# Performance work log

Measured on AMD Instinct MI355X. Metric: run time of the kernel, lower is better.

The kernel has to match this reference:

```python
import jax, jax.numpy as jnp
import numpy as np

D = 512       # hidden_size (attention defaults hardcode 512)
N = 8         # num_heads
H = D // N    # depth per head = 64
FF = 2048     # FFN filter size (hardcoded)
EPS = 1e-6


def _layer_norm(x, gamma, beta):
    # matches functional layer_norm: biased variance, eps inside sqrt
    mean = jnp.mean(x, axis=-1, keepdims=True)
    var = jnp.mean((x - mean) ** 2, axis=-1, keepdims=True)
    return gamma * ((x - mean) / jnp.sqrt(var + EPS)) + beta


def setup_inputs() -> dict:
    key = jax.random.key(0)
    ks = jax.random.split(key, 12)
    B, S = 8, 1024
    s = lambda k, shape, scale: jax.random.normal(k, shape, jnp.float32) * scale
    return {
        "inputs": s(ks[0], (B, S, D), 1.0),
        "attention_bias": jnp.zeros((B, 1, 1, S), jnp.float32),
        "ln1_g": jnp.ones((D,), jnp.float32),
        "ln1_b": jnp.zeros((D,), jnp.float32),
        "wq": s(ks[1], (D, N, H), D ** -0.5),
        "wk": s(ks[2], (D, N, H), D ** -0.5),
        "wv": s(ks[3], (D, N, H), D ** -0.5),
        "wo": s(ks[4], (N, H, D), D ** -0.5),
        "ln2_g": jnp.ones((D,), jnp.float32),
        "ln2_b": jnp.zeros((D,), jnp.float32),
        "w1": s(ks[5], (D, FF), D ** -0.5),
        "b1": jnp.zeros((FF,), jnp.float32),
        "w2": s(ks[6], (FF, D), FF ** -0.5),
        "b2": jnp.zeros((D,), jnp.float32),
    }


def reference(inputs, attention_bias, ln1_g, ln1_b, wq, wk, wv, wo,
              ln2_g, ln2_b, w1, b1, w2, b2):
    # --- self-attention block (pre-LN, residual) ---
    y = _layer_norm(inputs, ln1_g, ln1_b)
    q = jnp.einsum('bsd,dnh->bsnh', y, wq) * (H ** -0.5)
    k = jnp.einsum('bsd,dnh->bsnh', y, wk)
    v = jnp.einsum('bsd,dnh->bsnh', y, wv)
    # logits[b,n,f,t] = sum_h k[b,t,n,h] * q[b,f,n,h]
    logits = jnp.einsum('btnh,bfnh->bnft', k, q) + attention_bias
    weights = jax.nn.softmax(logits, axis=3)
    attn = jnp.einsum('bnft,btnh->bfnh', weights, v)
    attn_out = jnp.einsum('bfnh,nhd->bfd', attn, wo)
    x = inputs + attn_out

    # --- FFN block (pre-LN, residual) ---
    y2 = _layer_norm(x, ln2_g, ln2_b)
    h = jax.nn.relu(jnp.einsum('bsd,df->bsf', y2, w1) + b1)
    ffn_out = jnp.einsum('bsf,fd->bsd', h, w2) + b2
    return x + ffn_out
```

## Files before the change

### kernel.cpp

```cpp
#include <hip/hip_runtime.h>
#include <stdint.h>

typedef unsigned short u16;
typedef __attribute__((ext_vector_type(8))) __bf16 bf16x8;
typedef __attribute__((ext_vector_type(4))) float f32x4;

__device__ __forceinline__ float bf2f(u16 u) {
    union { unsigned int i; float f; } c; c.i = ((unsigned int)u) << 16; return c.f;
}
__device__ __forceinline__ u16 f2bf(float f) {
    union { float f; unsigned int i; } c; c.f = f;
    unsigned int u = c.i;
    u += 0x7FFFu + ((u >> 16) & 1u);
    return (u16)(u >> 16);
}
__device__ __forceinline__ bool sniff_f32(const unsigned* probe) {
    return probe && ((*probe & 0xFFFFu) == 0u);
}
__device__ __forceinline__ float lde(const void* p, size_t i, bool isf32) {
    return isf32 ? ((const float*)p)[i] : bf2f(((const u16*)p)[i]);
}
__device__ __forceinline__ void g2lds16(const void* g, void* l) {
    __builtin_amdgcn_global_load_lds(
        (__attribute__((address_space(1))) void*)(uintptr_t)g,
        (__attribute__((address_space(3))) void*)(unsigned int)(uintptr_t)l,
        16, 0, 0);
}

__global__ void prep_weights(const void* __restrict__ wq, const void* __restrict__ wk,
                             const void* __restrict__ wv, const void* __restrict__ wo,
                             const void* __restrict__ w1, const void* __restrict__ w2,
                             u16* __restrict__ wqkvT, u16* __restrict__ woT,
                             u16* __restrict__ w1T, u16* __restrict__ w2T,
                             const unsigned* probe) {
    __shared__ u16 t[32][33];
    const bool isf32 = sniff_f32(probe);
    const int id = blockIdx.x;
    const void* src; u16* dst; int R, C, cb, rb; float scale = 1.f;
    if (id < 1024) {
        const int which = id >> 8, tl = id & 255;
        R = 512; C = 512; cb = (tl & 15) * 32; rb = (tl >> 4) * 32;
        if (which == 0)      { src = wq; dst = wqkvT;              scale = 0.125f; }
        else if (which == 1) { src = wk; dst = wqkvT + 512 * 512; }
        else if (which == 2) { src = wv; dst = wqkvT + 1024 * 512; }
        else                 { src = wo; dst = woT; }
    } else if (id < 2048) {
        const int tl = id - 1024; src = w1; dst = w1T; R = 512; C = 2048;
        cb = (tl & 63) * 32; rb = (tl >> 6) * 32;
    } else {
        const int tl = id - 2048; src = w2; dst = w2T; R = 2048; C = 512;
        cb = (tl & 15) * 32; rb = (tl >> 4) * 32;
    }
    const int tx = threadIdx.x, ty = threadIdx.y;
#pragma unroll
    for (int i = 0; i < 4; i++)
        t[ty + i * 8][tx] = f2bf(lde(src, (size_t)(rb + ty + i * 8) * C + cb + tx, isf32));
    __syncthreads();
#pragma unroll
    for (int i = 0; i < 4; i++) {
        float v = bf2f(t[tx][ty + i * 8]) * scale;
        dst[(size_t)(cb + ty + i * 8) * R + rb + tx] = f2bf(v);
    }
}

__global__ __launch_bounds__(256) void ln_any(const void* __restrict__ x,
                                              const void* __restrict__ gw,
                                              const void* __restrict__ bw,
                                              u16* __restrict__ y,
                                              const unsigned* probe_x,
                                              const unsigned* probe_gb) {
    const bool xf32 = sniff_f32(probe_x);
    const bool gf32 = sniff_f32(probe_gb);
    const int lane = threadIdx.x & 63, wave = threadIdx.x >> 6;
    const int r = blockIdx.x * 4 + wave;
    union U8 { uint4 v; u16 s[8]; };
    float xs[8];
    if (xf32) {
        const float4* xr = (const float4*)((const float*)x + (size_t)r * 512 + lane * 8);
        float4 p0 = xr[0], p1 = xr[1];
        xs[0]=p0.x; xs[1]=p0.y; xs[2]=p0.z; xs[3]=p0.w;
        xs[4]=p1.x; xs[5]=p1.y; xs[6]=p1.z; xs[7]=p1.w;
    } else {
        U8 xu; xu.v = *(const uint4*)((const u16*)x + (size_t)r * 512 + lane * 8);
#pragma unroll
        for (int j = 0; j < 8; j++) xs[j] = bf2f(xu.s[j]);
    }
    float s1 = 0.f, s2 = 0.f;
#pragma unroll
    for (int j = 0; j < 8; j++) { s1 += xs[j]; s2 += xs[j] * xs[j]; }
#pragma unroll
    for (int d = 1; d < 64; d <<= 1) { s1 += __shfl_xor(s1, d); s2 += __shfl_xor(s2, d); }
    const float mean = s1 * (1.f / 512.f);
    const float var = s2 * (1.f / 512.f) - mean * mean;
    const float rstd = rsqrtf(var + 1e-6f);
    float gs[8], bs[8];
    if (gf32) {
        const float4* gr = (const float4*)((const float*)gw + lane * 8);
        const float4* br = (const float4*)((const float*)bw + lane * 8);
        float4 g0 = gr[0], g1 = gr[1], b0 = br[0], b1 = br[1];
        gs[0]=g0.x; gs[1]=g0.y; gs[2]=g0.z; gs[3]=g0.w; gs[4]=g1.x; gs[5]=g1.y; gs[6]=g1.z; gs[7]=g1.w;
        bs[0]=b0.x; bs[1]=b0.y; bs[2]=b0.z; bs[3]=b0.w; bs[4]=b1.x; bs[5]=b1.y; bs[6]=b1.z; bs[7]=b1.w;
    } else {
        U8 gu; gu.v = *(const uint4*)((const u16*)gw + lane * 8);
        U8 bu; bu.v = *(const uint4*)((const u16*)bw + lane * 8);
#pragma unroll
        for (int j = 0; j < 8; j++) { gs[j] = bf2f(gu.s[j]); bs[j] = bf2f(bu.s[j]); }
    }
    union U8 ou;
#pragma unroll
    for (int j = 0; j < 8; j++)
        ou.s[j] = f2bf(gs[j] * ((xs[j] - mean) * rstd) + bs[j]);
    *(uint4*)(y + (size_t)r * 512 + lane * 8) = ou.v;
}

template <int EPI>
__global__ __launch_bounds__(256, 2) void gemm_bt(const u16* __restrict__ A,
                                                  const u16* __restrict__ Bt,
                                                  const void* __restrict__ bias,
                                                  const void* __restrict__ res,
                                                  void* __restrict__ out,
                                                  u16* __restrict__ out2,
                                                  const unsigned* probe,
                                                  int M, int N, int K) {
    __shared__ __align__(16) u16 lA[128 * 32];
    __shared__ __align__(16) u16 lB[128 * 32];
    const int tid = threadIdx.x, wave = tid >> 6, lane = tid & 63;
    const int m0 = blockIdx.x * 128, n0 = blockIdx.y * 128;
    const int wm = (wave >> 1) * 64, wn = (wave & 1) * 64;
    const int row = lane & 15, quad = lane >> 4;
    f32x4 acc[4][4];
#pragma unroll
    for (int i = 0; i < 4; i++)
#pragma unroll
        for (int j = 0; j < 4; j++) acc[i][j] = (f32x4){0.f, 0.f, 0.f, 0.f};
    const u16* Ab = A + (size_t)m0 * K;
    const u16* Bb = Bt + (size_t)n0 * K;
    const int ch0 = wave, ch1 = wave + 4;
    const int e0 = ch0 * 64 + lane, e1 = ch1 * 64 + lane;
    const int r0 = e0 >> 2, c0 = (e0 & 3) * 8;
    const int r1 = e1 >> 2, c1 = (e1 & 3) * 8;
    for (int k0 = 0; k0 < K; k0 += 32) {
        __syncthreads();
        g2lds16(Ab + (size_t)r0 * K + k0 + c0, (char*)lA + ch0 * 1024);
        g2lds16(Bb + (size_t)r0 * K + k0 + c0, (char*)lB + ch0 * 1024);
        g2lds16(Ab + (size_t)r1 * K + k0 + c1, (char*)lA + ch1 * 1024);
        g2lds16(Bb + (size_t)r1 * K + k0 + c1, (char*)lB + ch1 * 1024);
        __syncthreads();
        bf16x8 af[4], bfr[4];
#pragma unroll
        for (int t = 0; t < 4; t++) {
            af[t]  = *(const bf16x8*)(lA + (wm + t * 16 + row) * 32 + quad * 8);
            bfr[t] = *(const bf16x8*)(lB + (wn + t * 16 + row) * 32 + quad * 8);
        }
#pragma unroll
        for (int i = 0; i < 4; i++)
#pragma unroll
            for (int j = 0; j < 4; j++)
                acc[i][j] = __builtin_amdgcn_mfma_f32_16x16x32_bf16(af[i], bfr[j], acc[i][j], 0, 0, 0);
    }
    const bool isf32 = sniff_f32(probe);
#pragma unroll
    for (int i = 0; i < 4; i++) {
        const int gm = m0 + wm + i * 16 + quad * 4;
#pragma unroll
        for (int j = 0; j < 4; j++) {
            const int gn = n0 + wn + j * 16 + row;
            float bv = 0.f;
            if (EPI == 2 || EPI == 3) bv = lde(bias, gn, isf32);
#pragma unroll
            for (int r = 0; r < 4; r++) {
                float v = acc[i][j][r];
                const int gmr = gm + r;
                size_t idx = (size_t)gmr * N + gn;
                if (EPI == 1) {
                    ((u16*)out)[idx] = f2bf(v + lde(res, idx, isf32));
                } else if (EPI == 2) {
                    v += bv;
                    ((u16*)out)[idx] = f2bf(v > 0.f ? v : 0.f);
                } else if (EPI == 3) {
                    v += bv + bf2f(((const u16*)res)[idx]);
                    if (isf32) ((float*)out)[idx] = v;
                    else       ((u16*)out)[idx] = f2bf(v);
                } else {
                    if (gn < 1024) {
                        ((u16*)out)[(size_t)gmr * 1024 + gn] = f2bf(v);
                    } else {
                        const int j2 = gn - 1024, n = j2 >> 6, h2 = j2 & 63;
                        const int b = gmr >> 10, t = gmr & 1023;
                        out2[(((size_t)b * 8 + n) * 64 + h2) * 1024 + t] = f2bf(v);
                    }
                }
            }
        }
    }
}

__global__ __launch_bounds__(256, 2) void attn_fused(const u16* __restrict__ qk,
                                                     const u16* __restrict__ vT,
                                                     const void* __restrict__ biasp,
                                                     u16* __restrict__ attn,
                                                     const unsigned* probe) {
    __shared__ __align__(16) u16 lQ[64 * 64];
    __shared__ __align__(16) u16 lK[128 * 64];
    __shared__ __align__(16) u16 lV[64 * 128];
    const bool isf32 = sniff_f32(probe);
    const int tid = threadIdx.x, wave = tid >> 6, lane = tid & 63;
    const int row = lane & 15, quad = lane >> 4;
    const int bn = blockIdx.x, b = bn >> 3, n = bn & 7;
    const int f0 = blockIdx.y * 64;
    const u16* Qg = qk + (size_t)(b * 1024 + f0) * 1024 + n * 64;
    const u16* Kg = qk + (size_t)(b * 1024) * 1024 + 512 + n * 64;
    const u16* Vg = vT + (size_t)bn * 65536;

#pragma unroll
    for (int j = 0; j < 2; j++) {
        const int ch = wave * 2 + j, e = ch * 64 + lane;
        const int rq = e >> 3, cq = ((e & 7) ^ (rq & 7)) * 8;
        g2lds16(Qg + (size_t)rq * 1024 + cq, (char*)lQ + ch * 1024);
    }
    float m_i = -1e30f, l_i = 0.f;
    f32x4 oacc[4];
#pragma unroll
    for (int h = 0; h < 4; h++) oacc[h] = (f32x4){0.f, 0.f, 0.f, 0.f};

    for (int t0 = 0; t0 < 1024; t0 += 128) {
        __syncthreads();
#pragma unroll
        for (int j = 0; j < 4; j++) {
            const int ch = wave * 4 + j, e = ch * 64 + lane;
            const int rk = e >> 3, ck = ((e & 7) ^ (rk & 7)) * 8;
            g2lds16(Kg + (size_t)(t0 + rk) * 1024 + ck, (char*)lK + ch * 1024);
            const int rv = e >> 4, cv = ((e & 15) ^ (rv & 7)) * 8;
            g2lds16(Vg + (size_t)rv * 1024 + t0 + cv, (char*)lV + ch * 1024);
        }
        __syncthreads();
        f32x4 s[8];
#pragma unroll
        for (int nt = 0; nt < 8; nt++) s[nt] = (f32x4){0.f, 0.f, 0.f, 0.f};
        const int fr = wave * 16 + row;
        bf16x8 bq[2];
#pragma unroll
        for (int ks = 0; ks < 2; ks++)
            bq[ks] = *(const bf16x8*)(lQ + fr * 64 + (((ks * 4 + quad) ^ (fr & 7)) * 8));
#pragma unroll
        for (int nt = 0; nt < 8; nt++) {
            const int tr = nt * 16 + row;
#pragma unroll
            for (int ks = 0; ks < 2; ks++) {
                bf16x8 ak = *(const bf16x8*)(lK + tr * 64 + (((ks * 4 + quad) ^ (tr & 7)) * 8));
                s[nt] = __builtin_amdgcn_mfma_f32_16x16x32_bf16(ak, bq[ks], s[nt], 0, 0, 0);
            }
        }
        float mx = -1e30f;
#pragma unroll
        for (int nt = 0; nt < 8; nt++) {
            const size_t bidx = (size_t)b * 1024 + t0 + nt * 16 + quad * 4;
            float bv4[4];
            if (isf32) {
                float4 t4 = *(const float4*)((const float*)biasp + bidx);
                bv4[0] = t4.x; bv4[1] = t4.y; bv4[2] = t4.z; bv4[3] = t4.w;
            } else {
                union { uint2 v; u16 s[4]; } bu;
                bu.v = *(const uint2*)((const u16*)biasp + bidx);
#pragma unroll
                for (int r = 0; r < 4; r++) bv4[r] = bf2f(bu.s[r]);
            }
#pragma unroll
            for (int r = 0; r < 4; r++) {
                s[nt][r] += bv4[r];
                mx = fmaxf(mx, s[nt][r]);
            }
        }
        mx = fmaxf(mx, __shfl_xor(mx, 16));
        mx = fmaxf(mx, __shfl_xor(mx, 32));
        const float mn = fmaxf(m_i, mx);
        const float alpha = __expf(m_i - mn);
        float rs = 0.f;
#pragma unroll
        for (int nt = 0; nt < 8; nt++)
#pragma unroll
            for (int r = 0; r < 4; r++) {
                float p = __expf(s[nt][r] - mn);
                s[nt][r] = p;
                rs += p;
            }
        rs += __shfl_xor(rs, 16);
        rs += __shfl_xor(rs, 32);
        l_i = l_i * alpha + rs;
        m_i = mn;
#pragma unroll
        for (int h = 0; h < 4; h++)
#pragma unroll
            for (int r = 0; r < 4; r++) oacc[h][r] *= alpha;
#pragma unroll
        for (int ks = 0; ks < 4; ks++) {
            unsigned pw[4];
#pragma unroll
            for (int g = 0; g < 2; g++) {
                pw[g * 2 + 0] = (unsigned)f2bf(s[ks * 2 + g][0]) | ((unsigned)f2bf(s[ks * 2 + g][1]) << 16);
                pw[g * 2 + 1] = (unsigned)f2bf(s[ks * 2 + g][2]) | ((unsigned)f2bf(s[ks * 2 + g][3]) << 16);
            }
            union { unsigned u[4]; bf16x8 v8; } bb;
#pragma unroll
            for (int w = 0; w < 4; w++) {
                const int srcl = ((((quad & 1) << 1) | (w >> 1)) << 4) | row;
                const unsigned lo = (unsigned)__shfl((int)pw[(w & 1)], srcl);
                const unsigned hi = (unsigned)__shfl((int)pw[2 + (w & 1)], srcl);
                bb.u[w] = (quad & 2) ? hi : lo;
            }
#pragma unroll
            for (int ht = 0; ht < 4; ht++) {
                const int vr = ht * 16 + row;
                bf16x8 av = *(const bf16x8*)(lV + vr * 128 + (((ks * 4 + quad) ^ (vr & 7)) * 8));
                oacc[ht] = __builtin_amdgcn_mfma_f32_16x16x32_bf16(av, bb.v8, oacc[ht], 0, 0, 0);
            }
        }
    }
    const float inv = 1.f / l_i;
    const int f = f0 + wave * 16 + row;
#pragma unroll
    for (int ht = 0; ht < 4; ht++) {
        uint2 ov;
        ov.x = (unsigned)f2bf(oacc[ht][0] * inv) | ((unsigned)f2bf(oacc[ht][1] * inv) << 16);
        ov.y = (unsigned)f2bf(oacc[ht][2] * inv) | ((unsigned)f2bf(oacc[ht][3] * inv) << 16);
        *(uint2*)(attn + (size_t)(b * 1024 + f) * 512 + n * 64 + ht * 16 + quad * 4) = ov;
    }
}

extern "C" void kernel_launch(void* const* d_in, const int* in_sizes, int n_in,
                              void* d_out, int out_size, void* d_ws, size_t ws_size,
                              hipStream_t stream) {
    const void* inp  = d_in[0];
    const void* ab   = d_in[1];
    const void* ln1g = d_in[2];
    const void* ln1b = d_in[3];
    const void* wq   = d_in[4];
    const void* wk   = d_in[5];
    const void* wv   = d_in[6];
    const void* wo   = d_in[7];
    const void* ln2g = d_in[8];
    const void* ln2b = d_in[9];
    const void* w1   = d_in[10];
    const void* b1   = d_in[11];
    const void* w2   = d_in[12];
    const void* b2   = d_in[13];
    const unsigned* probe = (const unsigned*)d_in[2];

    char* ws = (char*)d_ws;
    size_t off = 0;
    auto alloc = [&](size_t bytes) -> void* { void* p = ws + off; off += bytes; return p; };
    u16* wqkvT = (u16*)alloc(1536 * 512 * 2);
    u16* woT   = (u16*)alloc(512 * 512 * 2);
    u16* w1T   = (u16*)alloc(2048 * 512 * 2);
    u16* w2T   = (u16*)alloc(512 * 2048 * 2);
    u16* ybuf  = (u16*)alloc((size_t)8192 * 512 * 2);
    u16* qk    = (u16*)alloc((size_t)8192 * 1024 * 2);
    u16* vT    = (u16*)alloc((size_t)64 * 64 * 1024 * 2);
    u16* attn  = (u16*)alloc((size_t)8192 * 512 * 2);
    u16* xbf   = (u16*)alloc((size_t)8192 * 512 * 2);
    u16* hbuf  = qk;

    prep_weights<<<3072, dim3(32, 8), 0, stream>>>(wq, wk, wv, wo, w1, w2,
                                                   wqkvT, woT, w1T, w2T, probe);
    ln_any<<<2048, 256, 0, stream>>>(inp, ln1g, ln1b, ybuf, probe, probe);
    gemm_bt<4><<<dim3(64, 12), 256, 0, stream>>>(ybuf, wqkvT, nullptr, nullptr, qk, vT, nullptr, 8192, 1536, 512);
    attn_fused<<<dim3(64, 16), 256, 0, stream>>>(qk, vT, ab, attn, probe);
    gemm_bt<1><<<dim3(64, 4), 256, 0, stream>>>(attn, woT, nullptr, inp, xbf, nullptr, probe, 8192, 512, 512);
    ln_any<<<2048, 256, 0, stream>>>(xbf, ln2g, ln2b, ybuf, nullptr, probe);
    gemm_bt<2><<<dim3(64, 16), 256, 0, stream>>>(ybuf, w1T, b1, nullptr, hbuf, nullptr, probe, 8192, 2048, 512);
    gemm_bt<3><<<dim3(64, 4), 256, 0, stream>>>(hbuf, w2T, b2, xbf, (u16*)d_out, nullptr, probe, 8192, 512, 2048);
}
```

Before: 280.6 us.

## Double-buffer GEMM LDS tiles and use 64-row tiles for N=512 GEMMs

```diff
diff --git a/kernel.cpp b/kernel.cpp
--- a/kernel.cpp
+++ b/kernel.cpp
@@ -113,7 +113,7 @@
     *(uint4*)(y + (size_t)r * 512 + lane * 8) = ou.v;
 }
 
-template <int EPI>
+template <int EPI, int TM>
 __global__ __launch_bounds__(256, 2) void gemm_bt(const u16* __restrict__ A,
                                                   const u16* __restrict__ Bt,
                                                   const void* __restrict__ bias,
@@ -122,45 +122,61 @@
                                                   u16* __restrict__ out2,
                                                   const unsigned* probe,
                                                   int M, int N, int K) {
-    __shared__ __align__(16) u16 lA[128 * 32];
-    __shared__ __align__(16) u16 lB[128 * 32];
+    constexpr int ACH = TM / 16;
+    constexpr int MI = TM / 32;
+    __shared__ __align__(16) u16 lA[2][TM * 32];
+    __shared__ __align__(16) u16 lB[2][128 * 32];
     const int tid = threadIdx.x, wave = tid >> 6, lane = tid & 63;
-    const int m0 = blockIdx.x * 128, n0 = blockIdx.y * 128;
-    const int wm = (wave >> 1) * 64, wn = (wave & 1) * 64;
+    const int m0 = blockIdx.x * TM, n0 = blockIdx.y * 128;
+    const int wm = (wave >> 1) * (TM / 2), wn = (wave & 1) * 64;
     const int row = lane & 15, quad = lane >> 4;
-    f32x4 acc[4][4];
-#pragma unroll
-    for (int i = 0; i < 4; i++)
+    f32x4 acc[MI][4];
+#pragma unroll
+    for (int i = 0; i < MI; i++)
 #pragma unroll
         for (int j = 0; j < 4; j++) acc[i][j] = (f32x4){0.f, 0.f, 0.f, 0.f};
     const u16* Ab = A + (size_t)m0 * K;
     const u16* Bb = Bt + (size_t)n0 * K;
-    const int ch0 = wave, ch1 = wave + 4;
-    const int e0 = ch0 * 64 + lane, e1 = ch1 * 64 + lane;
-    const int r0 = e0 >> 2, c0 = (e0 & 3) * 8;
-    const int r1 = e1 >> 2, c1 = (e1 & 3) * 8;
+
+    auto stage = [&](int buf, int k0) {
+#pragma unroll
+        for (int c = 0; c < (ACH + 8 + 3) / 4; c++) {
+            const int ch = c * 4 + wave;
+            if (ch < ACH) {
+                const int e = ch * 64 + lane;
+                const int r = e >> 2, col = (e & 3) * 8;
+                g2lds16(Ab + (size_t)r * K + k0 + col, (char*)lA[buf] + ch * 1024);
+            } else if (ch < ACH + 8) {
+                const int c2 = ch - ACH;
+                const int e = c2 * 64 + lane;
+                const int r = e >> 2, col = (e & 3) * 8;
+                g2lds16(Bb + (size_t)r * K + k0 + col, (char*)lB[buf] + c2 * 1024);
+            }
+        }
+    };
+
+    stage(0, 0);
+    int cur = 0;
     for (int k0 = 0; k0 < K; k0 += 32) {
         __syncthreads();
-        g2lds16(Ab + (size_t)r0 * K + k0 + c0, (char*)lA + ch0 * 1024);
-        g2lds16(Bb + (size_t)r0 * K + k0 + c0, (char*)lB + ch0 * 1024);
-        g2lds16(Ab + (size_t)r1 * K + k0 + c1, (char*)lA + ch1 * 1024);
-        g2lds16(Bb + (size_t)r1 * K + k0 + c1, (char*)lB + ch1 * 1024);
-        __syncthreads();
-        bf16x8 af[4], bfr[4];
-#pragma unroll
-        for (int t = 0; t < 4; t++) {
-            af[t]  = *(const bf16x8*)(lA + (wm + t * 16 + row) * 32 + quad * 8);
-            bfr[t] = *(const bf16x8*)(lB + (wn + t * 16 + row) * 32 + quad * 8);
-        }
-#pragma unroll
-        for (int i = 0; i < 4; i++)
+        if (k0 + 32 < K) stage(cur ^ 1, k0 + 32);
+        bf16x8 af[MI], bfr[4];
+#pragma unroll
+        for (int t = 0; t < MI; t++)
+            af[t]  = *(const bf16x8*)(lA[cur] + (wm + t * 16 + row) * 32 + quad * 8);
+#pragma unroll
+        for (int t = 0; t < 4; t++)
+            bfr[t] = *(const bf16x8*)(lB[cur] + (wn + t * 16 + row) * 32 + quad * 8);
+#pragma unroll
+        for (int i = 0; i < MI; i++)
 #pragma unroll
             for (int j = 0; j < 4; j++)
                 acc[i][j] = __builtin_amdgcn_mfma_f32_16x16x32_bf16(af[i], bfr[j], acc[i][j], 0, 0, 0);
+        cur ^= 1;
     }
     const bool isf32 = sniff_f32(probe);
 #pragma unroll
-    for (int i = 0; i < 4; i++) {
+    for (int i = 0; i < MI; i++) {
         const int gm = m0 + wm + i * 16 + quad * 4;
 #pragma unroll
         for (int j = 0; j < 4; j++) {
@@ -363,10 +379,10 @@
     prep_weights<<<3072, dim3(32, 8), 0, stream>>>(wq, wk, wv, wo, w1, w2,
                                                    wqkvT, woT, w1T, w2T, probe);
     ln_any<<<2048, 256, 0, stream>>>(inp, ln1g, ln1b, ybuf, probe, probe);
-    gemm_bt<4><<<dim3(64, 12), 256, 0, stream>>>(ybuf, wqkvT, nullptr, nullptr, qk, vT, nullptr, 8192, 1536, 512);
+    gemm_bt<4, 128><<<dim3(64, 12), 256, 0, stream>>>(ybuf, wqkvT, nullptr, nullptr, qk, vT, nullptr, 8192, 1536, 512);
     attn_fused<<<dim3(64, 16), 256, 0, stream>>>(qk, vT, ab, attn, probe);
-    gemm_bt<1><<<dim3(64, 4), 256, 0, stream>>>(attn, woT, nullptr, inp, xbf, nullptr, probe, 8192, 512, 512);
+    gemm_bt<1, 64><<<dim3(128, 4), 256, 0, stream>>>(attn, woT, nullptr, inp, xbf, nullptr, probe, 8192, 512, 512);
     ln_any<<<2048, 256, 0, stream>>>(xbf, ln2g, ln2b, ybuf, nullptr, probe);
-    gemm_bt<2><<<dim3(64, 16), 256, 0, stream>>>(ybuf, w1T, b1, nullptr, hbuf, nullptr, probe, 8192, 2048, 512);
-    gemm_bt<3><<<dim3(64, 4), 256, 0, stream>>>(hbuf, w2T, b2, xbf, (u16*)d_out, nullptr, probe, 8192, 512, 2048);
-}
+    gemm_bt<2, 128><<<dim3(64, 16), 256, 0, stream>>>(ybuf, w1T, b1, nullptr, hbuf, nullptr, probe, 8192, 2048, 512);
+    gemm_bt<3, 64><<<dim3(128, 4), 256, 0, stream>>>(hbuf, w2T, b2, xbf, (u16*)d_out, nullptr, probe, 8192, 512, 2048);
+}
```

Measured after the change: 258.9 us. 7.7% less time.
